# Kernel tuning notes

Hardware: AMD Instinct MI355X
Metric: run time of the kernel (lower is better)

## Reference

```python
import jax, jax.numpy as jnp
import numpy as np

N = 100000      # nodes
NE = 1250000    # edges
D = 64          # in_dim == out_dim
H = 8           # heads
DH = D // H     # per-head dim


def setup_inputs() -> dict:
    key = jax.random.key(0)
    ks = jax.random.split(key, 7)
    s = 1.0 / np.sqrt(D)
    return {
        "x": jax.random.normal(ks[0], (N, D), jnp.float32),
        "edge_attr": jax.random.normal(ks[1], (NE, D), jnp.float32),
        "WQ": jax.random.normal(ks[2], (D, D), jnp.float32) * s,
        "WK": jax.random.normal(ks[3], (D, D), jnp.float32) * s,
        "WV": jax.random.normal(ks[4], (D, D), jnp.float32) * s,
        "WE": jax.random.normal(ks[5], (D, D), jnp.float32) * s,
        "edge_index": jax.random.randint(ks[6], (2, NE), 0, N, dtype=jnp.int32),
    }


def reference(x, edge_attr, WQ, WK, WV, WE, edge_index):
    # Linear projections (torch Linear y = x W^T; here W is stored [in,out])
    Q = (x @ WQ).reshape(N, H, DH)
    K = (x @ WK).reshape(N, H, DH)
    V = (x @ WV).reshape(N, H, DH)
    Ef = (edge_attr @ WE).reshape(NE, H, DH)

    src = edge_index[0]
    dst = edge_index[1]

    # per-edge score: exp(clamp(sum_d K[src]*Q[dst]*E / sqrt(DH), -5, 5))
    score = (K[src] * Q[dst]) * (1.0 / np.sqrt(DH)) * Ef  # [E,H,DH]
    score = jnp.exp(jnp.clip(score.sum(-1, keepdims=True), -5.0, 5.0))  # [E,H,1]

    msg = V[src] * score  # [E,H,DH]
    wV = jax.ops.segment_sum(msg, dst, num_segments=N)    # [N,H,DH]
    Z = jax.ops.segment_sum(score, dst, num_segments=N)   # [N,H,1]

    h_out = wV / (Z + 1e-6)
    return h_out.reshape(N, H * DH)
```

## Files before the change

### kernel.cpp

```cpp
#include <hip/hip_runtime.h>
#include <hip/hip_bf16.h>

#define NN    100000
#define NEDGE 1250000

typedef __attribute__((ext_vector_type(8))) short bf16x8;
typedef __attribute__((ext_vector_type(8))) unsigned short u16x8;
typedef __attribute__((ext_vector_type(4))) float f32x4;

__device__ __forceinline__ short f2bf(float f) {
    unsigned u = __float_as_uint(f);
    u += 0x7FFFu + ((u >> 16) & 1u);
    return (short)(u >> 16);
}
__device__ __forceinline__ float bf2f(unsigned short u) {
    return __uint_as_float(((unsigned)u) << 16);
}

constexpr size_t OFF_Q    = 0;
constexpr size_t OFF_KB   = OFF_Q    + (size_t)NN * 64 * 4;
constexpr size_t OFF_VB   = OFF_KB   + (size_t)NN * 64 * 2;
constexpr size_t OFF_SRT  = OFF_VB   + (size_t)NN * 64 * 2;
constexpr size_t OFF_HIST = OFF_SRT  + (size_t)NEDGE * 8;
constexpr size_t OFF_EX   = OFF_HIST + (size_t)NN * 4;
constexpr size_t OFF_BSUM = OFF_EX   + (size_t)NN * 4;
constexpr size_t OFF_BOFF = OFF_BSUM + 512 * 4;
constexpr size_t OFF_START= OFF_BOFF + 512 * 4;
constexpr size_t OFF_CUR  = OFF_START+ (size_t)(NN + 1) * 4;
constexpr size_t WS_NEED  = OFF_CUR  + (size_t)NN * 4;
constexpr int NB_SCAN = (NN + 255) / 256;

__global__ __launch_bounds__(256) void qkv_kernel(
    const float* __restrict__ x,
    const float* __restrict__ WQ, const float* __restrict__ WK,
    const float* __restrict__ WV,
    float* __restrict__ Qf, unsigned short* __restrict__ Kb,
    unsigned short* __restrict__ Vb)
{
    const int lane = threadIdx.x & 63;
    const int wid  = threadIdx.x >> 6;
    const int gw   = blockIdx.x * 4 + wid;
    const int nw   = gridDim.x * 4;
    const int colb = lane & 15;
    const int krow = (lane >> 4) * 8;

    bf16x8 Bf[3][4][2];
    const float* Ws[3] = {WQ, WK, WV};
    #pragma unroll
    for (int m = 0; m < 3; ++m)
        #pragma unroll
        for (int n = 0; n < 4; ++n)
            #pragma unroll
            for (int kh = 0; kh < 2; ++kh) {
                bf16x8 b;
                #pragma unroll
                for (int j = 0; j < 8; ++j)
                    b[j] = f2bf(Ws[m][(size_t)(kh * 32 + krow + j) * 64 + n * 16 + colb]);
                Bf[m][n][kh] = b;
            }

    for (int tile = gw; tile < NN / 16; tile += nw) {
        const int r0 = tile * 16;
        const float* xr = x + (size_t)(r0 + colb) * 64 + krow;
        f32x4 a0 = *(const f32x4*)(xr);
        f32x4 a1 = *(const f32x4*)(xr + 4);
        f32x4 a2 = *(const f32x4*)(xr + 32);
        f32x4 a3 = *(const f32x4*)(xr + 36);
        bf16x8 Alo, Ahi;
        #pragma unroll
        for (int j = 0; j < 4; ++j) {
            Alo[j]     = f2bf(a0[j]);
            Alo[4 + j] = f2bf(a1[j]);
            Ahi[j]     = f2bf(a2[j]);
            Ahi[4 + j] = f2bf(a3[j]);
        }
        #pragma unroll
        for (int m = 0; m < 3; ++m) {
            #pragma unroll
            for (int n = 0; n < 4; ++n) {
                f32x4 acc = {0.f, 0.f, 0.f, 0.f};
                acc = __builtin_amdgcn_mfma_f32_16x16x32_bf16(Alo, Bf[m][n][0], acc, 0, 0, 0);
                acc = __builtin_amdgcn_mfma_f32_16x16x32_bf16(Ahi, Bf[m][n][1], acc, 0, 0, 0);
                #pragma unroll
                for (int q = 0; q < 4; ++q) {
                    const size_t idx = (size_t)(r0 + (lane >> 4) * 4 + q) * 64 + n * 16 + colb;
                    if (m == 0)      Qf[idx] = acc[q];
                    else if (m == 1) Kb[idx] = (unsigned short)f2bf(acc[q]);
                    else             Vb[idx] = (unsigned short)f2bf(acc[q]);
                }
            }
        }
    }
}

__global__ void zero_hist_kernel(int* __restrict__ hist) {
    const int i = blockIdx.x * blockDim.x + threadIdx.x;
    if (i < NN) hist[i] = 0;
}

__global__ void hist_kernel(const int* __restrict__ ei, int* __restrict__ hist) {
    const int e = blockIdx.x * blockDim.x + threadIdx.x;
    if (e < NEDGE) atomicAdd(&hist[ei[NEDGE + e]], 1);
}

__global__ __launch_bounds__(256) void scanA_kernel(
    const int* __restrict__ hist, int* __restrict__ ex, int* __restrict__ bsum)
{
    __shared__ int wsum[4];
    const int i = blockIdx.x * 256 + threadIdx.x;
    const int lane = threadIdx.x & 63, wid = threadIdx.x >> 6;
    const int v = (i < NN) ? hist[i] : 0;
    int incl = v;
    #pragma unroll
    for (int off = 1; off < 64; off <<= 1) {
        int t = __shfl_up(incl, off);
        if (lane >= off) incl += t;
    }
    if (lane == 63) wsum[wid] = incl;
    __syncthreads();
    int pre = 0, bt = 0;
    #pragma unroll
    for (int w = 0; w < 4; ++w) { int s = wsum[w]; bt += s; if (w < wid) pre += s; }
    if (i < NN) ex[i] = incl - v + pre;
    if (threadIdx.x == 0) bsum[blockIdx.x] = bt;
}

__global__ __launch_bounds__(512) void scanB_kernel(
    const int* __restrict__ bsum, int* __restrict__ boff)
{
    __shared__ int wsum[8];
    const int i = threadIdx.x;
    const int lane = i & 63, wid = i >> 6;
    const int v = (i < NB_SCAN) ? bsum[i] : 0;
    int incl = v;
    #pragma unroll
    for (int off = 1; off < 64; off <<= 1) {
        int t = __shfl_up(incl, off);
        if (lane >= off) incl += t;
    }
    if (lane == 63) wsum[wid] = incl;
    __syncthreads();
    int pre = 0;
    #pragma unroll
    for (int w = 0; w < 8; ++w) { if (w < wid) pre += wsum[w]; }
    if (i < NB_SCAN) boff[i] = incl - v + pre;
}

__global__ void scanC_kernel(const int* __restrict__ ex, const int* __restrict__ boff,
                             int* __restrict__ start, int* __restrict__ cursor)
{
    const int i = blockIdx.x * blockDim.x + threadIdx.x;
    if (i < NN) {
        const int s = ex[i] + boff[i >> 8];
        start[i] = s;
        cursor[i] = s;
    } else if (i == NN) {
        start[NN] = NEDGE;
    }
}

__global__ void scatter_kernel(const int* __restrict__ ei, int* __restrict__ cursor,
                               int2* __restrict__ sorted)
{
    const int e = blockIdx.x * blockDim.x + threadIdx.x;
    if (e < NEDGE) {
        const int dst = ei[NEDGE + e];
        const int pos = atomicAdd(&cursor[dst], 1);
        sorted[pos] = make_int2(ei[e], e);
    }
}

__global__ __launch_bounds__(256) void agg_kernel(
    const float* __restrict__ Qn, const unsigned short* __restrict__ Kb,
    const unsigned short* __restrict__ Vb,
    const float* __restrict__ edge_attr, const float* __restrict__ WE,
    const int* __restrict__ start, const int2* __restrict__ sorted,
    float* __restrict__ out)
{
    const int lane = threadIdx.x & 63;
    const int wid  = threadIdx.x >> 6;
    const int gw   = (blockIdx.x * blockDim.x + threadIdx.x) >> 6;
    const int nw   = (gridDim.x * blockDim.x) >> 6;
    const int colb = lane & 15;
    const int krow = (lane >> 4) * 8;
    const int el   = lane >> 3;
    const int h    = lane & 7;
    const float c  = 0.35355339059327373f;

    __shared__ float efs_all[4][16][68];
    float (*efs)[68] = efs_all[wid];

    bf16x8 Bf[4][2];
    #pragma unroll
    for (int n = 0; n < 4; ++n)
        #pragma unroll
        for (int kh = 0; kh < 2; ++kh) {
            bf16x8 b;
            #pragma unroll
            for (int j = 0; j < 8; ++j)
                b[j] = f2bf(WE[(size_t)(kh * 32 + krow + j) * 64 + n * 16 + colb]);
            Bf[n][kh] = b;
        }

    int dst = gw;
    int beg = 0, end = 0;
    int2 se = make_int2(0, 0);
    f32x4 a0 = {0,0,0,0}, a1 = {0,0,0,0}, a2 = {0,0,0,0}, a3 = {0,0,0,0};
    if (dst < NN) {
        beg = start[dst]; end = start[dst + 1];
        int rpos = beg + colb;
        if (rpos >= end) rpos = beg;
        if (rpos >= NEDGE) rpos = NEDGE - 1;
        se = sorted[rpos];
        const float* ear = edge_attr + (size_t)se.y * 64 + krow;
        a0 = *(const f32x4*)(ear);
        a1 = *(const f32x4*)(ear + 4);
        a2 = *(const f32x4*)(ear + 32);
        a3 = *(const f32x4*)(ear + 36);
    }

    for (; dst < NN; dst += nw) {
        const int dn = dst + nw;
        int beg_n = 0, end_n = 0;
        if (dn < NN) { beg_n = start[dn]; end_n = start[dn + 1]; }

        const int s0 = __shfl(se.x, el);
        const int s1 = __shfl(se.x, el + 8);
        const u16x8 k0v = *(const u16x8*)(Kb + (size_t)s0 * 64 + h * 8);
        const u16x8 v0v = *(const u16x8*)(Vb + (size_t)s0 * 64 + h * 8);
        const u16x8 k1v = *(const u16x8*)(Kb + (size_t)s1 * 64 + h * 8);
        const u16x8 v1v = *(const u16x8*)(Vb + (size_t)s1 * 64 + h * 8);
        const float* qp = Qn + (size_t)dst * 64 + h * 8;
        const f32x4 q0 = *(const f32x4*)(qp);
        const f32x4 q1 = *(const f32x4*)(qp + 4);

        bf16x8 Alo, Ahi;
        #pragma unroll
        for (int jj = 0; jj < 4; ++jj) {
            Alo[jj]     = f2bf(a0[jj]);
            Alo[4 + jj] = f2bf(a1[jj]);
            Ahi[jj]     = f2bf(a2[jj]);
            Ahi[4 + jj] = f2bf(a3[jj]);
        }
        const int rbase = (lane >> 4) * 4;
        #pragma unroll
        for (int n = 0; n < 4; ++n) {
            f32x4 z = {0.f, 0.f, 0.f, 0.f};
            z = __builtin_amdgcn_mfma_f32_16x16x32_bf16(Alo, Bf[n][0], z, 0, 0, 0);
            z = __builtin_amdgcn_mfma_f32_16x16x32_bf16(Ahi, Bf[n][1], z, 0, 0, 0);
            #pragma unroll
            for (int q = 0; q < 4; ++q)
                efs[rbase + q][n * 16 + colb] = z[q];
        }

        int2 se_n = make_int2(0, 0);
        f32x4 a0n = {0,0,0,0}, a1n = {0,0,0,0}, a2n = {0,0,0,0}, a3n = {0,0,0,0};
        if (dn < NN) {
            int rpos_n = beg_n + colb;
            if (rpos_n >= end_n) rpos_n = beg_n;
            if (rpos_n >= NEDGE) rpos_n = NEDGE - 1;
            se_n = sorted[rpos_n];
            const float* earn = edge_attr + (size_t)se_n.y * 64 + krow;
            a0n = *(const f32x4*)(earn);
            a1n = *(const f32x4*)(earn + 4);
            a2n = *(const f32x4*)(earn + 32);
            a3n = *(const f32x4*)(earn + 36);
        }

        asm volatile("s_waitcnt lgkmcnt(0)" ::: "memory");
        __builtin_amdgcn_sched_barrier(0);

        f32x4 av0 = {0,0,0,0}, av1 = {0,0,0,0};
        float az = 0.f;
        {
            const f32x4 e00 = *(const f32x4*)(&efs[el][h * 8]);
            const f32x4 e01 = *(const f32x4*)(&efs[el][h * 8 + 4]);
            const f32x4 e10 = *(const f32x4*)(&efs[el + 8][h * 8]);
            const f32x4 e11 = *(const f32x4*)(&efs[el + 8][h * 8 + 4]);
            float t0 = 0.f, t1 = 0.f;
            #pragma unroll
            for (int d = 0; d < 4; ++d) {
                t0 += bf2f(k0v[d])     * q0[d] * e00[d];
                t0 += bf2f(k0v[4 + d]) * q1[d] * e01[d];
                t1 += bf2f(k1v[d])     * q0[d] * e10[d];
                t1 += bf2f(k1v[4 + d]) * q1[d] * e11[d];
            }
            const bool act0 = (beg + el)     < end;
            const bool act1 = (beg + el + 8) < end;
            const float sc0 = act0 ? __expf(fminf(fmaxf(t0 * c, -5.f), 5.f)) : 0.f;
            const float sc1 = act1 ? __expf(fminf(fmaxf(t1 * c, -5.f), 5.f)) : 0.f;
            az += sc0 + sc1;
            #pragma unroll
            for (int d = 0; d < 4; ++d) {
                av0[d] += bf2f(v0v[d])     * sc0 + bf2f(v1v[d])     * sc1;
                av1[d] += bf2f(v0v[4 + d]) * sc0 + bf2f(v1v[4 + d]) * sc1;
            }
        }

        for (int j = beg + 16; j < end; j += 16) {
            int rpos = j + colb;
            if (rpos >= end) rpos = beg;
            const int2 seb = sorted[rpos];
            const int sb0 = __shfl(seb.x, el);
            const int sb1 = __shfl(seb.x, el + 8);
            const u16x8 kb0 = *(const u16x8*)(Kb + (size_t)sb0 * 64 + h * 8);
            const u16x8 vb0 = *(const u16x8*)(Vb + (size_t)sb0 * 64 + h * 8);
            const u16x8 kb1 = *(const u16x8*)(Kb + (size_t)sb1 * 64 + h * 8);
            const u16x8 vb1 = *(const u16x8*)(Vb + (size_t)sb1 * 64 + h * 8);
            const float* earb = edge_attr + (size_t)seb.y * 64 + krow;
            const f32x4 b0 = *(const f32x4*)(earb);
            const f32x4 b1 = *(const f32x4*)(earb + 4);
            const f32x4 b2 = *(const f32x4*)(earb + 32);
            const f32x4 b3 = *(const f32x4*)(earb + 36);
            bf16x8 Blo, Bhi;
            #pragma unroll
            for (int jj = 0; jj < 4; ++jj) {
                Blo[jj]     = f2bf(b0[jj]);
                Blo[4 + jj] = f2bf(b1[jj]);
                Bhi[jj]     = f2bf(b2[jj]);
                Bhi[4 + jj] = f2bf(b3[jj]);
            }
            #pragma unroll
            for (int n = 0; n < 4; ++n) {
                f32x4 z = {0.f, 0.f, 0.f, 0.f};
                z = __builtin_amdgcn_mfma_f32_16x16x32_bf16(Blo, Bf[n][0], z, 0, 0, 0);
                z = __builtin_amdgcn_mfma_f32_16x16x32_bf16(Bhi, Bf[n][1], z, 0, 0, 0);
                #pragma unroll
                for (int q = 0; q < 4; ++q)
                    efs[rbase + q][n * 16 + colb] = z[q];
            }
            asm volatile("s_waitcnt lgkmcnt(0)" ::: "memory");
            __builtin_amdgcn_sched_barrier(0);
            const f32x4 e00 = *(const f32x4*)(&efs[el][h * 8]);
            const f32x4 e01 = *(const f32x4*)(&efs[el][h * 8 + 4]);
            const f32x4 e10 = *(const f32x4*)(&efs[el + 8][h * 8]);
            const f32x4 e11 = *(const f32x4*)(&efs[el + 8][h * 8 + 4]);
            float t0 = 0.f, t1 = 0.f;
            #pragma unroll
            for (int d = 0; d < 4; ++d) {
                t0 += bf2f(kb0[d])     * q0[d] * e00[d];
                t0 += bf2f(kb0[4 + d]) * q1[d] * e01[d];
                t1 += bf2f(kb1[d])     * q0[d] * e10[d];
                t1 += bf2f(kb1[4 + d]) * q1[d] * e11[d];
            }
            const bool act0 = (j + el)     < end;
            const bool act1 = (j + el + 8) < end;
            const float sc0 = act0 ? __expf(fminf(fmaxf(t0 * c, -5.f), 5.f)) : 0.f;
            const float sc1 = act1 ? __expf(fminf(fmaxf(t1 * c, -5.f), 5.f)) : 0.f;
            az += sc0 + sc1;
            #pragma unroll
            for (int d = 0; d < 4; ++d) {
                av0[d] += bf2f(vb0[d])     * sc0 + bf2f(vb1[d])     * sc1;
                av1[d] += bf2f(vb0[4 + d]) * sc0 + bf2f(vb1[4 + d]) * sc1;
            }
        }

        #pragma unroll
        for (int off = 8; off < 64; off <<= 1) {
            az += __shfl_xor(az, off);
            #pragma unroll
            for (int d = 0; d < 4; ++d) {
                av0[d] += __shfl_xor(av0[d], off);
                av1[d] += __shfl_xor(av1[d], off);
            }
        }

        if (el == 0) {
            const float inv = 1.f / (az + 1e-6f);
            f32x4 o0, o1;
            #pragma unroll
            for (int d = 0; d < 4; ++d) { o0[d] = av0[d] * inv; o1[d] = av1[d] * inv; }
            float* op = out + (size_t)dst * 64 + h * 8;
            *(f32x4*)(op)     = o0;
            *(f32x4*)(op + 4) = o1;
        }

        beg = beg_n; end = end_n; se = se_n;
        a0 = a0n; a1 = a1n; a2 = a2n; a3 = a3n;
    }
}

__global__ __launch_bounds__(256) void edge_kernel_fb(
    const float* __restrict__ edge_attr, const float* __restrict__ WE,
    const float* __restrict__ Qn, const unsigned short* __restrict__ Kb,
    const unsigned short* __restrict__ Vb, const int* __restrict__ ei,
    float* __restrict__ outAcc, float* __restrict__ Z)
{
    const int lane = threadIdx.x & 63;
    const int wid  = threadIdx.x >> 6;
    const int gw   = blockIdx.x * 4 + wid;
    const int nw   = gridDim.x * 4;
    const int colb = lane & 15;
    const int krow = (lane >> 4) * 8;
    const int b8   = (lane >> 3) & 1;

    bf16x8 Bf[4][2];
    #pragma unroll
    for (int n = 0; n < 4; ++n)
        #pragma unroll
        for (int kh = 0; kh < 2; ++kh) {
            bf16x8 b;
            #pragma unroll
            for (int j = 0; j < 8; ++j)
                b[j] = f2bf(WE[(size_t)(kh * 32 + krow + j) * 64 + n * 16 + colb]);
            Bf[n][kh] = b;
        }

    const float inv_sqrt_dh = 0.35355339059327373f;

    for (int tile = gw; tile < NEDGE / 16; tile += nw) {
        const int e0 = tile * 16;
        const float* ear = edge_attr + (size_t)(e0 + colb) * 64 + krow;
        f32x4 a0 = *(const f32x4*)(ear);
        f32x4 a1 = *(const f32x4*)(ear + 4);
        f32x4 a2 = *(const f32x4*)(ear + 32);
        f32x4 a3 = *(const f32x4*)(ear + 36);
        bf16x8 Alo, Ahi;
        #pragma unroll
        for (int j = 0; j < 4; ++j) {
            Alo[j]     = f2bf(a0[j]);
            Alo[4 + j] = f2bf(a1[j]);
            Ahi[j]     = f2bf(a2[j]);
            Ahi[4 + j] = f2bf(a3[j]);
        }
        f32x4 acc[4];
        #pragma unroll
        for (int n = 0; n < 4; ++n) {
            f32x4 z = {0.f, 0.f, 0.f, 0.f};
            z = __builtin_amdgcn_mfma_f32_16x16x32_bf16(Alo, Bf[n][0], z, 0, 0, 0);
            z = __builtin_amdgcn_mfma_f32_16x16x32_bf16(Ahi, Bf[n][1], z, 0, 0, 0);
            acc[n] = z;
        }
        int srcq[4], dstq[4];
        #pragma unroll
        for (int q = 0; q < 4; ++q) {
            const int erl = (lane >> 4) * 4 + q;
            srcq[q] = ei[e0 + erl];
            dstq[q] = ei[NEDGE + e0 + erl];
        }
        float sc[4][4];
        #pragma unroll
        for (int q = 0; q < 4; ++q) {
            #pragma unroll
            for (int n = 0; n < 4; ++n) {
                const int cidx = n * 16 + colb;
                const float kv = bf2f(Kb[(size_t)srcq[q] * 64 + cidx]);
                const float qv = Qn[(size_t)dstq[q] * 64 + cidx];
                float t = kv * qv * acc[n][q];
                t += __shfl_xor(t, 1);
                t += __shfl_xor(t, 2);
                t += __shfl_xor(t, 4);
                const float s = fminf(fmaxf(t * inv_sqrt_dh, -5.0f), 5.0f);
                sc[q][n] = __expf(s);
            }
        }
        #pragma unroll
        for (int q = 0; q < 4; ++q) {
            #pragma unroll
            for (int n = 0; n < 4; ++n) {
                const int cidx = n * 16 + colb;
                const float vv = bf2f(Vb[(size_t)srcq[q] * 64 + cidx]);
                unsafeAtomicAdd(&outAcc[(size_t)dstq[q] * 64 + cidx], vv * sc[q][n]);
                if ((lane & 7) == 0) {
                    const int hh = 2 * n + b8;
                    unsafeAtomicAdd(&Z[(size_t)dstq[q] * 8 + hh], sc[q][n]);
                }
            }
        }
    }
}

__global__ void finalize_fb(float* __restrict__ out, const float* __restrict__ Z) {
    const int i = blockIdx.x * blockDim.x + threadIdx.x;
    if (i < NN * 64) {
        const int node = i >> 6;
        const int h    = (i >> 3) & 7;
        out[i] = out[i] / (Z[node * 8 + h] + 1e-6f);
    }
}

extern "C" void kernel_launch(void* const* d_in, const int* in_sizes, int n_in,
                              void* d_out, int out_size, void* d_ws, size_t ws_size,
                              hipStream_t stream) {
    const float* x         = (const float*)d_in[0];
    const float* edge_attr = (const float*)d_in[1];
    const float* WQ        = (const float*)d_in[2];
    const float* WK        = (const float*)d_in[3];
    const float* WV        = (const float*)d_in[4];
    const float* WE        = (const float*)d_in[5];
    const int*   ei        = (const int*)d_in[6];
    float* out = (float*)d_out;

    char* base = (char*)d_ws;
    float*          Qf = (float*)(base + OFF_Q);
    unsigned short* Kb = (unsigned short*)(base + OFF_KB);
    unsigned short* Vb = (unsigned short*)(base + OFF_VB);

    qkv_kernel<<<1563, 256, 0, stream>>>(x, WQ, WK, WV, Qf, Kb, Vb);

    if (ws_size >= WS_NEED) {
        int2* sorted = (int2*)(base + OFF_SRT);
        int* hist    = (int*)(base + OFF_HIST);
        int* ex      = (int*)(base + OFF_EX);
        int* bsum    = (int*)(base + OFF_BSUM);
        int* boff    = (int*)(base + OFF_BOFF);
        int* start   = (int*)(base + OFF_START);
        int* cursor  = (int*)(base + OFF_CUR);

        zero_hist_kernel<<<NB_SCAN, 256, 0, stream>>>(hist);
        hist_kernel<<<(NEDGE + 255) / 256, 256, 0, stream>>>(ei, hist);
        scanA_kernel<<<NB_SCAN, 256, 0, stream>>>(hist, ex, bsum);
        scanB_kernel<<<1, 512, 0, stream>>>(bsum, boff);
        scanC_kernel<<<(NN + 256) / 256 + 1, 256, 0, stream>>>(ex, boff, start, cursor);
        scatter_kernel<<<(NEDGE + 255) / 256, 256, 0, stream>>>(ei, cursor, sorted);
        agg_kernel<<<4096, 256, 0, stream>>>(Qf, Kb, Vb, edge_attr, WE, start, sorted, out);
    } else {
        float* Z = (float*)(base + OFF_SRT);
        hipMemsetAsync(d_out, 0, (size_t)NN * 64 * sizeof(float), stream);
        hipMemsetAsync(Z, 0, (size_t)NN * 8 * sizeof(float), stream);
        edge_kernel_fb<<<2048, 256, 0, stream>>>(edge_attr, WE, Qf, Kb, Vb, ei, out, Z);
        finalize_fb<<<(NN * 64 + 255) / 256, 256, 0, stream>>>(out, Z);
    }
}
```

Measured before the change: 319.3 us.

## Store Q in bf16, fold hist zeroing into QKV, merge scan stages

Q is now stored as bf16 instead of fp32, which halves Q write traffic in the projection kernel and Q read traffic in aggregation. Histogram zeroing moves into the QKV kernel, and the single-block scanB kernel is removed: each scanC block now sums the preceding block totals itself. Together these remove two kernel launches. In exchange Q loses precision, and each scan block redundantly reads up to about 391 partial sums.

```diff
diff --git a/kernel.cpp b/kernel.cpp
--- a/kernel.cpp
+++ b/kernel.cpp
@@ -17,15 +17,14 @@
     return __uint_as_float(((unsigned)u) << 16);
 }
 
-constexpr size_t OFF_Q    = 0;
-constexpr size_t OFF_KB   = OFF_Q    + (size_t)NN * 64 * 4;
+constexpr size_t OFF_QB   = 0;
+constexpr size_t OFF_KB   = OFF_QB   + (size_t)NN * 64 * 2;
 constexpr size_t OFF_VB   = OFF_KB   + (size_t)NN * 64 * 2;
 constexpr size_t OFF_SRT  = OFF_VB   + (size_t)NN * 64 * 2;
 constexpr size_t OFF_HIST = OFF_SRT  + (size_t)NEDGE * 8;
 constexpr size_t OFF_EX   = OFF_HIST + (size_t)NN * 4;
 constexpr size_t OFF_BSUM = OFF_EX   + (size_t)NN * 4;
-constexpr size_t OFF_BOFF = OFF_BSUM + 512 * 4;
-constexpr size_t OFF_START= OFF_BOFF + 512 * 4;
+constexpr size_t OFF_START= OFF_BSUM + 512 * 4;
 constexpr size_t OFF_CUR  = OFF_START+ (size_t)(NN + 1) * 4;
 constexpr size_t WS_NEED  = OFF_CUR  + (size_t)NN * 4;
 constexpr int NB_SCAN = (NN + 255) / 256;
@@ -34,9 +33,15 @@
     const float* __restrict__ x,
     const float* __restrict__ WQ, const float* __restrict__ WK,
     const float* __restrict__ WV,
-    float* __restrict__ Qf, unsigned short* __restrict__ Kb,
-    unsigned short* __restrict__ Vb)
+    unsigned short* __restrict__ Qb, unsigned short* __restrict__ Kb,
+    unsigned short* __restrict__ Vb, int* __restrict__ hist)
 {
+    if (hist) {
+        for (int i = blockIdx.x * blockDim.x + threadIdx.x; i < NN;
+             i += gridDim.x * blockDim.x)
+            hist[i] = 0;
+    }
+
     const int lane = threadIdx.x & 63;
     const int wid  = threadIdx.x >> 6;
     const int gw   = blockIdx.x * 4 + wid;
@@ -58,6 +63,8 @@
                     b[j] = f2bf(Ws[m][(size_t)(kh * 32 + krow + j) * 64 + n * 16 + colb]);
                 Bf[m][n][kh] = b;
             }
+
+    unsigned short* Outs[3] = {Qb, Kb, Vb};
 
     for (int tile = gw; tile < NN / 16; tile += nw) {
         const int r0 = tile * 16;
@@ -82,20 +89,12 @@
                 acc = __builtin_amdgcn_mfma_f32_16x16x32_bf16(Alo, Bf[m][n][0], acc, 0, 0, 0);
                 acc = __builtin_amdgcn_mfma_f32_16x16x32_bf16(Ahi, Bf[m][n][1], acc, 0, 0, 0);
                 #pragma unroll
-                for (int q = 0; q < 4; ++q) {
-                    const size_t idx = (size_t)(r0 + (lane >> 4) * 4 + q) * 64 + n * 16 + colb;
-                    if (m == 0)      Qf[idx] = acc[q];
-                    else if (m == 1) Kb[idx] = (unsigned short)f2bf(acc[q]);
-                    else             Vb[idx] = (unsigned short)f2bf(acc[q]);
-                }
-            }
-        }
-    }
-}
-
-__global__ void zero_hist_kernel(int* __restrict__ hist) {
-    const int i = blockIdx.x * blockDim.x + threadIdx.x;
-    if (i < NN) hist[i] = 0;
+                for (int q = 0; q < 4; ++q)
+                    Outs[m][(size_t)(r0 + (lane >> 4) * 4 + q) * 64 + n * 16 + colb] =
+                        (unsigned short)f2bf(acc[q]);
+            }
+        }
+    }
 }
 
 __global__ void hist_kernel(const int* __restrict__ ei, int* __restrict__ hist) {
@@ -125,33 +124,24 @@
     if (threadIdx.x == 0) bsum[blockIdx.x] = bt;
 }
 
-__global__ __launch_bounds__(512) void scanB_kernel(
-    const int* __restrict__ bsum, int* __restrict__ boff)
+__global__ __launch_bounds__(256) void scanC_kernel(
+    const int* __restrict__ ex, const int* __restrict__ bsum,
+    int* __restrict__ start, int* __restrict__ cursor)
 {
-    __shared__ int wsum[8];
-    const int i = threadIdx.x;
-    const int lane = i & 63, wid = i >> 6;
-    const int v = (i < NB_SCAN) ? bsum[i] : 0;
-    int incl = v;
-    #pragma unroll
-    for (int off = 1; off < 64; off <<= 1) {
-        int t = __shfl_up(incl, off);
-        if (lane >= off) incl += t;
-    }
-    if (lane == 63) wsum[wid] = incl;
+    __shared__ int sboff;
+    const int b   = blockIdx.x;
+    const int tid = threadIdx.x;
+    if (tid < 64) {
+        int p = 0;
+        for (int j = tid; j < b; j += 64) p += bsum[j];
+        #pragma unroll
+        for (int off = 32; off >= 1; off >>= 1) p += __shfl_down(p, off);
+        if (tid == 0) sboff = p;
+    }
     __syncthreads();
-    int pre = 0;
-    #pragma unroll
-    for (int w = 0; w < 8; ++w) { if (w < wid) pre += wsum[w]; }
-    if (i < NB_SCAN) boff[i] = incl - v + pre;
-}
-
-__global__ void scanC_kernel(const int* __restrict__ ex, const int* __restrict__ boff,
-                             int* __restrict__ start, int* __restrict__ cursor)
-{
-    const int i = blockIdx.x * blockDim.x + threadIdx.x;
+    const int i = b * 256 + tid;
     if (i < NN) {
-        const int s = ex[i] + boff[i >> 8];
+        const int s = ex[i] + sboff;
         start[i] = s;
         cursor[i] = s;
     } else if (i == NN) {
@@ -171,7 +161,7 @@
 }
 
 __global__ __launch_bounds__(256) void agg_kernel(
-    const float* __restrict__ Qn, const unsigned short* __restrict__ Kb,
+    const unsigned short* __restrict__ Qb, const unsigned short* __restrict__ Kb,
     const unsigned short* __restrict__ Vb,
     const float* __restrict__ edge_attr, const float* __restrict__ WE,
     const int* __restrict__ start, const int2* __restrict__ sorted,
@@ -210,7 +200,7 @@
         beg = start[dst]; end = start[dst + 1];
         int rpos = beg + colb;
         if (rpos >= end) rpos = beg;
-        if (rpos >= NEDGE) rpos = NEDGE - 1;
+        if (rpos >= NEDGE) rpos = 0;
         se = sorted[rpos];
         const float* ear = edge_attr + (size_t)se.y * 64 + krow;
         a0 = *(const f32x4*)(ear);
@@ -230,9 +220,7 @@
         const u16x8 v0v = *(const u16x8*)(Vb + (size_t)s0 * 64 + h * 8);
         const u16x8 k1v = *(const u16x8*)(Kb + (size_t)s1 * 64 + h * 8);
         const u16x8 v1v = *(const u16x8*)(Vb + (size_t)s1 * 64 + h * 8);
-        const float* qp = Qn + (size_t)dst * 64 + h * 8;
-        const f32x4 q0 = *(const f32x4*)(qp);
-        const f32x4 q1 = *(const f32x4*)(qp + 4);
+        const u16x8 qv  = *(const u16x8*)(Qb + (size_t)dst * 64 + h * 8);
 
         bf16x8 Alo, Ahi;
         #pragma unroll
@@ -258,7 +246,7 @@
         if (dn < NN) {
             int rpos_n = beg_n + colb;
             if (rpos_n >= end_n) rpos_n = beg_n;
-            if (rpos_n >= NEDGE) rpos_n = NEDGE - 1;
+            if (rpos_n >= NEDGE) rpos_n = 0;
             se_n = sorted[rpos_n];
             const float* earn = edge_attr + (size_t)se_n.y * 64 + krow;
             a0n = *(const f32x4*)(earn);
@@ -269,6 +257,10 @@
 
         asm volatile("s_waitcnt lgkmcnt(0)" ::: "memory");
         __builtin_amdgcn_sched_barrier(0);
+
+        f32x4 q0, q1;
+        #pragma unroll
+        for (int d = 0; d < 4; ++d) { q0[d] = bf2f(qv[d]); q1[d] = bf2f(qv[4 + d]); }
 
         f32x4 av0 = {0,0,0,0}, av1 = {0,0,0,0};
         float az = 0.f;
@@ -308,17 +300,17 @@
             const u16x8 kb1 = *(const u16x8*)(Kb + (size_t)sb1 * 64 + h * 8);
             const u16x8 vb1 = *(const u16x8*)(Vb + (size_t)sb1 * 64 + h * 8);
             const float* earb = edge_attr + (size_t)seb.y * 64 + krow;
-            const f32x4 b0 = *(const f32x4*)(earb);
-            const f32x4 b1 = *(const f32x4*)(earb + 4);
-            const f32x4 b2 = *(const f32x4*)(earb + 32);
-            const f32x4 b3 = *(const f32x4*)(earb + 36);
+            const f32x4 c0 = *(const f32x4*)(earb);
+            const f32x4 c1 = *(const f32x4*)(earb + 4);
+            const f32x4 c2 = *(const f32x4*)(earb + 32);
+            const f32x4 c3 = *(const f32x4*)(earb + 36);
             bf16x8 Blo, Bhi;
             #pragma unroll
             for (int jj = 0; jj < 4; ++jj) {
-                Blo[jj]     = f2bf(b0[jj]);
-                Blo[4 + jj] = f2bf(b1[jj]);
-                Bhi[jj]     = f2bf(b2[jj]);
-                Bhi[4 + jj] = f2bf(b3[jj]);
+                Blo[jj]     = f2bf(c0[jj]);
+                Blo[4 + jj] = f2bf(c1[jj]);
+                Bhi[jj]     = f2bf(c2[jj]);
+                Bhi[4 + jj] = f2bf(c3[jj]);
             }
             #pragma unroll
             for (int n = 0; n < 4; ++n) {
@@ -382,7 +374,7 @@
 
 __global__ __launch_bounds__(256) void edge_kernel_fb(
     const float* __restrict__ edge_attr, const float* __restrict__ WE,
-    const float* __restrict__ Qn, const unsigned short* __restrict__ Kb,
+    const unsigned short* __restrict__ Qb, const unsigned short* __restrict__ Kb,
     const unsigned short* __restrict__ Vb, const int* __restrict__ ei,
     float* __restrict__ outAcc, float* __restrict__ Z)
 {
@@ -445,7 +437,7 @@
             for (int n = 0; n < 4; ++n) {
                 const int cidx = n * 16 + colb;
                 const float kv = bf2f(Kb[(size_t)srcq[q] * 64 + cidx]);
-                const float qv = Qn[(size_t)dstq[q] * 64 + cidx];
+                const float qv = bf2f(Qb[(size_t)dstq[q] * 64 + cidx]);
                 float t = kv * qv * acc[n][q];
                 t += __shfl_xor(t, 1);
                 t += __shfl_xor(t, 2);
@@ -492,33 +484,30 @@
     float* out = (float*)d_out;
 
     char* base = (char*)d_ws;
-    float*          Qf = (float*)(base + OFF_Q);
+    unsigned short* Qb = (unsigned short*)(base + OFF_QB);
     unsigned short* Kb = (unsigned short*)(base + OFF_KB);
     unsigned short* Vb = (unsigned short*)(base + OFF_VB);
-
-    qkv_kernel<<<1563, 256, 0, stream>>>(x, WQ, WK, WV, Qf, Kb, Vb);
 
     if (ws_size >= WS_NEED) {
         int2* sorted = (int2*)(base + OFF_SRT);
         int* hist    = (int*)(base + OFF_HIST);
         int* ex      = (int*)(base + OFF_EX);
         int* bsum    = (int*)(base + OFF_BSUM);
-        int* boff    = (int*)(base + OFF_BOFF);
         int* start   = (int*)(base + OFF_START);
         int* cursor  = (int*)(base + OFF_CUR);
 
-        zero_hist_kernel<<<NB_SCAN, 256, 0, stream>>>(hist);
+        qkv_kernel<<<1563, 256, 0, stream>>>(x, WQ, WK, WV, Qb, Kb, Vb, hist);
         hist_kernel<<<(NEDGE + 255) / 256, 256, 0, stream>>>(ei, hist);
         scanA_kernel<<<NB_SCAN, 256, 0, stream>>>(hist, ex, bsum);
-        scanB_kernel<<<1, 512, 0, stream>>>(bsum, boff);
-        scanC_kernel<<<(NN + 256) / 256 + 1, 256, 0, stream>>>(ex, boff, start, cursor);
+        scanC_kernel<<<NB_SCAN, 256, 0, stream>>>(ex, bsum, start, cursor);
         scatter_kernel<<<(NEDGE + 255) / 256, 256, 0, stream>>>(ei, cursor, sorted);
-        agg_kernel<<<4096, 256, 0, stream>>>(Qf, Kb, Vb, edge_attr, WE, start, sorted, out);
+        agg_kernel<<<4096, 256, 0, stream>>>(Qb, Kb, Vb, edge_attr, WE, start, sorted, out);
     } else {
         float* Z = (float*)(base + OFF_SRT);
+        qkv_kernel<<<1563, 256, 0, stream>>>(x, WQ, WK, WV, Qb, Kb, Vb, nullptr);
         hipMemsetAsync(d_out, 0, (size_t)NN * 64 * sizeof(float), stream);
         hipMemsetAsync(Z, 0, (size_t)NN * 8 * sizeof(float), stream);
-        edge_kernel_fb<<<2048, 256, 0, stream>>>(edge_attr, WE, Qf, Kb, Vb, ei, out, Z);
+        edge_kernel_fb<<<2048, 256, 0, stream>>>(edge_attr, WE, Qb, Kb, Vb, ei, out, Z);
         finalize_fb<<<(NN * 64 + 255) / 256, 256, 0, stream>>>(out, Z);
     }
 }
```

Measured after the change: 315.5 us. Within noise of the previous version (-1.2%).
